# Optimization experiments

Hardware: AMD Instinct MI355X
Metric: run time of the kernel (lower is better)

## Reference

```python
import jax, jax.numpy as jnp
import numpy as np

B, L, E, H = 4096, 200, 64, 128

def setup_inputs() -> dict:
    key = jax.random.key(0)
    k1, k2, k3, k4, k5, k6, k7 = jax.random.split(key, 7)
    behavior_emb = jax.random.normal(k1, (B, L, E), dtype=jnp.float32)
    target_emb = jax.random.normal(k2, (B, 1, E), dtype=jnp.float32)
    seq_len = jax.random.randint(k3, (B,), 0, 200)
    # attention MLP params: Linear(4E, H), Linear(H, 1)
    W1 = jax.random.normal(k4, (4 * E, H), dtype=jnp.float32) / np.sqrt(4 * E)
    b1 = jnp.zeros((H,), dtype=jnp.float32)
    W2 = jax.random.normal(k5, (H, 1), dtype=jnp.float32) / np.sqrt(H)
    b2 = jnp.zeros((1,), dtype=jnp.float32)
    return {"behavior_emb": behavior_emb, "target_emb": target_emb,
            "seq_len": seq_len, "W1": W1, "b1": b1, "W2": W2, "b2": b2}

def reference(behavior_emb, target_emb, seq_len, W1, b1, W2, b2):
    b, l, e = behavior_emb.shape
    t = jnp.broadcast_to(target_emb, (b, l, e))  # [B,L,E]
    # concat(behavior, target, behavior*target, behavior-target) -> [B,L,4E]
    feat = jnp.concatenate([behavior_emb, t, behavior_emb * t, behavior_emb - t], axis=-1)
    h = jax.nn.relu(jnp.einsum('blf,fh->blh', feat, W1) + b1)  # dropout = identity (eval)
    att = (jnp.einsum('blh,ho->blo', h, W2) + b2)[..., 0]      # [B,L]
    mask = jnp.arange(l)[None, :] < seq_len[:, None]           # [B,L]
    att = jnp.where(mask, att, -1e9)
    att = jax.nn.softmax(att, axis=-1)
    weighted_emb = jnp.einsum('bl,ble->be', att, behavior_emb)  # [B,E]
    return weighted_emb
```

## Files before the change

### kernel.cpp

```cpp
#include <hip/hip_runtime.h>
#include <hip/hip_bf16.h>

typedef __attribute__((ext_vector_type(8))) __bf16 bf16x8;
typedef __attribute__((ext_vector_type(4))) __bf16 bf16x4;
typedef __attribute__((ext_vector_type(4))) float  f32x4;

#define L_SEQ 200
#define LPAD  208

__global__ void setup_bc(const float* __restrict__ W1, __bf16* __restrict__ Bc) {
    const int idx = blockIdx.x * 256 + threadIdx.x;
    const int j  = idx & 7;
    const int c  = (idx >> 3) & 15;
    const int kq = (idx >> 7) & 3;
    const int ks = (idx >> 9) & 3;
    const int ct = idx >> 11;
    const int k   = ks * 32 + kq * 8 + j;
    const int col = ct * 16 + c;
    float v;
    if (k < 64) v = W1[k * 128 + col] + W1[(192 + k) * 128 + col];
    else        v = W1[(128 + (k - 64)) * 128 + col];
    Bc[idx] = (__bf16)v;
}

__global__ __launch_bounds__(256) void setup_tb(
    const float* __restrict__ target, const float* __restrict__ W1,
    const float* __restrict__ b1, __bf16* __restrict__ TB)
{
    __shared__ float Wbd[64][128];
    __shared__ float Ts[16][64];
    const int tid = threadIdx.x;
    const int b0  = blockIdx.x * 16;
    for (int q = tid; q < 64 * 128; q += 256) {
        const int e = q >> 7, c = q & 127;
        Wbd[e][c] = W1[(64 + e) * 128 + c] - W1[(192 + e) * 128 + c];
    }
    for (int q = tid; q < 16 * 64; q += 256) {
        const int bb = q >> 6, e = q & 63;
        Ts[bb][e] = target[(size_t)(b0 + bb) * 64 + e];
    }
    __syncthreads();
    const int bb = tid >> 4;
    const int c0 = (tid & 15) * 8;
    float acc[8];
    #pragma unroll
    for (int r = 0; r < 8; ++r) acc[r] = b1[c0 + r];
    for (int e = 0; e < 64; ++e) {
        const float tv = Ts[bb][e];
        #pragma unroll
        for (int r = 0; r < 8; ++r) acc[r] += tv * Wbd[e][c0 + r];
    }
    #pragma unroll
    for (int r = 0; r < 8; ++r)
        TB[(size_t)(b0 + bb) * 128 + c0 + r] = (__bf16)acc[r];
}

__global__ __launch_bounds__(256, 4) void din_main(
    const float* __restrict__ behavior,
    const float* __restrict__ target,
    const int*   __restrict__ seqlen,
    const float* __restrict__ W2,
    const __bf16* __restrict__ Bc,
    const __bf16* __restrict__ TB,
    float* __restrict__ out)
{
    __shared__ __align__(16) __bf16 Xbf[LPAD * 64];
    __shared__ float att_part[4][LPAD];
    __shared__ float att_s[LPAD];
    __shared__ float red_s[8];
    __shared__ float part_s[4 * 64];

    const int b    = blockIdx.x;
    const int tid  = threadIdx.x;
    const int lane = tid & 63;
    const int w    = tid >> 6;
    const int kq   = lane >> 4;
    const int c16  = lane & 15;

    bf16x8 bfrag[2][4];
    #pragma unroll
    for (int i = 0; i < 2; ++i) {
        const int ct = 2 * w + i;
        #pragma unroll
        for (int ks = 0; ks < 4; ++ks)
            bfrag[i][ks] = *(const bf16x8*)(Bc + ((ct * 4 + ks) * 4 + kq) * 128 + c16 * 8);
    }
    float tf0[8], tf1[8];
    {
        const float* tp = target + (size_t)b * 64 + kq * 8;
        #pragma unroll
        for (int j = 0; j < 8; ++j) { tf0[j] = tp[j]; tf1[j] = tp[32 + j]; }
    }
    float tb_l[2], w2_l[2];
    #pragma unroll
    for (int i = 0; i < 2; ++i) {
        const int col = (2 * w + i) * 16 + c16;
        tb_l[i] = (float)TB[(size_t)b * 128 + col];
        w2_l[i] = W2[col];
    }

    {
        const float4* Xg = (const float4*)(behavior + (size_t)b * L_SEQ * 64);
        for (int q = tid; q < L_SEQ * 16; q += 256) {
            const int row = q >> 4;
            const int j   = q & 15;
            float4 v = Xg[q];
            bf16x4 u = { (__bf16)v.x, (__bf16)v.y, (__bf16)v.z, (__bf16)v.w };
            *(bf16x4*)&Xbf[row * 64 + ((j * 4) ^ ((row & 7) << 3))] = u;
        }
        for (int q = tid; q < 8 * 64; q += 256) {
            const int row = L_SEQ + (q >> 6);
            const int e   = q & 63;
            Xbf[row * 64 + (e ^ ((row & 7) << 3))] = (__bf16)0.0f;
        }
    }
    __syncthreads();

    {
        const int k0 = kq * 8;
        for (int tile = 0; tile < 13; ++tile) {
            const int row = tile * 16 + c16;
            const int sw  = (row & 7) << 3;
            bf16x8 a0 = *(const bf16x8*)&Xbf[row * 64 + (k0 ^ sw)];
            bf16x8 a1 = *(const bf16x8*)&Xbf[row * 64 + ((k0 + 32) ^ sw)];
            bf16x8 a2, a3;
            #pragma unroll
            for (int j = 0; j < 8; ++j) {
                a2[j] = (__bf16)((float)a0[j] * tf0[j]);
                a3[j] = (__bf16)((float)a1[j] * tf1[j]);
            }
            float s[4] = {0.f, 0.f, 0.f, 0.f};
            #pragma unroll
            for (int i = 0; i < 2; ++i) {
                f32x4 acc = {0.f, 0.f, 0.f, 0.f};
                acc = __builtin_amdgcn_mfma_f32_16x16x32_bf16(a0, bfrag[i][0], acc, 0, 0, 0);
                acc = __builtin_amdgcn_mfma_f32_16x16x32_bf16(a1, bfrag[i][1], acc, 0, 0, 0);
                acc = __builtin_amdgcn_mfma_f32_16x16x32_bf16(a2, bfrag[i][2], acc, 0, 0, 0);
                acc = __builtin_amdgcn_mfma_f32_16x16x32_bf16(a3, bfrag[i][3], acc, 0, 0, 0);
                #pragma unroll
                for (int r = 0; r < 4; ++r)
                    s[r] += fmaxf(acc[r] + tb_l[i], 0.f) * w2_l[i];
            }
            #pragma unroll
            for (int r = 0; r < 4; ++r) {
                float v = s[r];
                v += __shfl_xor(v, 1, 64);
                v += __shfl_xor(v, 2, 64);
                v += __shfl_xor(v, 4, 64);
                v += __shfl_xor(v, 8, 64);
                s[r] = v;
            }
            if (c16 == 0) {
                const int r0 = tile * 16 + kq * 4;
                #pragma unroll
                for (int r = 0; r < 4; ++r) att_part[w][r0 + r] = s[r];
            }
        }
    }
    __syncthreads();

    {
        const int sl = seqlen[b];
        float val = -INFINITY;
        if (tid < L_SEQ) {
            float v = att_part[0][tid] + att_part[1][tid]
                    + att_part[2][tid] + att_part[3][tid];
            val = (tid < sl) ? v : -1e9f;
        }
        float m = val;
        #pragma unroll
        for (int d = 1; d < 64; d <<= 1) m = fmaxf(m, __shfl_xor(m, d, 64));
        if (lane == 0) red_s[w] = m;
        __syncthreads();
        m = fmaxf(fmaxf(red_s[0], red_s[1]), fmaxf(red_s[2], red_s[3]));
        float p = (tid < L_SEQ) ? __expf(val - m) : 0.f;
        float sum = p;
        #pragma unroll
        for (int d = 1; d < 64; d <<= 1) sum += __shfl_xor(sum, d, 64);
        if (lane == 0) red_s[4 + w] = sum;
        __syncthreads();
        sum = red_s[4] + red_s[5] + red_s[6] + red_s[7];
        const float winv = 1.0f / sum;
        if (tid < L_SEQ) att_s[tid] = p * winv;
    }
    __syncthreads();

    {
        float acc = 0.f;
        for (int l = w; l < L_SEQ; l += 4)
            acc += att_s[l] * (float)Xbf[l * 64 + (lane ^ ((l & 7) << 3))];
        part_s[w * 64 + lane] = acc;
    }
    __syncthreads();
    if (tid < 64)
        out[(size_t)b * 64 + tid] =
            part_s[tid] + part_s[64 + tid] + part_s[128 + tid] + part_s[192 + tid];
}

extern "C" void kernel_launch(void* const* d_in, const int* in_sizes, int n_in,
                              void* d_out, int out_size, void* d_ws, size_t ws_size,
                              hipStream_t stream) {
    (void)n_in; (void)out_size; (void)ws_size;
    const float* behavior = (const float*)d_in[0];
    const float* target   = (const float*)d_in[1];
    const int*   seqlen   = (const int*)d_in[2];
    const float* W1       = (const float*)d_in[3];
    const float* b1       = (const float*)d_in[4];
    const float* W2       = (const float*)d_in[5];
    float* out = (float*)d_out;
    const int B = in_sizes[2];

    __bf16* Bc = (__bf16*)d_ws;
    __bf16* TB = (__bf16*)((char*)d_ws + 32768);

    setup_bc<<<dim3(64), dim3(256), 0, stream>>>(W1, Bc);
    setup_tb<<<dim3(B / 16), dim3(256), 0, stream>>>(target, W1, b1, TB);
    din_main<<<dim3(B), dim3(256), 0, stream>>>(behavior, target, seqlen, W2, Bc, TB, out);
}
```

Measured before the change: 334.2 us.

## Fold target into per-batch effective weights to halve MFMA work

Precomputes a per-batch bf16 weight matrix Weff = (W_a+W_d) + t*W_c, so the main kernel multiplies behavior rows by a 64-wide K instead of 128 and no longer forms behavior*target in registers. It also issues behavior loads in batches before the shared-memory writes, prefetches the next MFMA A-fragments, raises the occupancy hint to 5, keeps TB in fp32, and vectorizes the weighted-sum pass with 8-wide LDS reads and shuffle reductions. In exchange, a per-batch weight tensor (16 KB per batch, 64 MB total) is written and read back through global memory, and the product term is now rounded differently.

```diff
diff --git a/kernel.cpp b/kernel.cpp
--- a/kernel.cpp
+++ b/kernel.cpp
@@ -3,29 +3,56 @@
 
 typedef __attribute__((ext_vector_type(8))) __bf16 bf16x8;
 typedef __attribute__((ext_vector_type(4))) __bf16 bf16x4;
+typedef __attribute__((ext_vector_type(2))) __bf16 bf16x2;
 typedef __attribute__((ext_vector_type(4))) float  f32x4;
 
 #define L_SEQ 200
 #define LPAD  208
 
-__global__ void setup_bc(const float* __restrict__ W1, __bf16* __restrict__ Bc) {
-    const int idx = blockIdx.x * 256 + threadIdx.x;
-    const int j  = idx & 7;
-    const int c  = (idx >> 3) & 15;
-    const int kq = (idx >> 7) & 3;
-    const int ks = (idx >> 9) & 3;
-    const int ct = idx >> 11;
-    const int k   = ks * 32 + kq * 8 + j;
-    const int col = ct * 16 + c;
-    float v;
-    if (k < 64) v = W1[k * 128 + col] + W1[(192 + k) * 128 + col];
-    else        v = W1[(128 + (k - 64)) * 128 + col];
-    Bc[idx] = (__bf16)v;
+__global__ __launch_bounds__(256) void setup_weff(
+    const float* __restrict__ W1, const float* __restrict__ target,
+    __bf16* __restrict__ Weff)
+{
+    __shared__ float t_s[16][64];
+    const int tid = threadIdx.x;
+    const int b0  = blockIdx.x * 16;
+    ((float4*)t_s)[tid] = ((const float4*)(target + (size_t)b0 * 64))[tid];
+
+    const int c16 = tid & 15;
+    const int kq  = (tid >> 4) & 3;
+    const int ks  = (tid >> 6) & 1;
+    const int k0  = ks * 32 + kq * 8;
+    float wad[4][8], wc[4][8];
+    #pragma unroll
+    for (int i = 0; i < 4; ++i) {
+        const int col = (i * 2 + (tid >> 7)) * 16 + c16;
+        #pragma unroll
+        for (int j = 0; j < 8; ++j) {
+            const int k = k0 + j;
+            wad[i][j] = W1[k * 128 + col] + W1[(192 + k) * 128 + col];
+            wc[i][j]  = W1[(128 + k) * 128 + col];
+        }
+    }
+    __syncthreads();
+    for (int bb = 0; bb < 16; ++bb) {
+        float tv[8];
+        #pragma unroll
+        for (int j = 0; j < 8; ++j) tv[j] = t_s[bb][k0 + j];
+        #pragma unroll
+        for (int i = 0; i < 4; ++i) {
+            const int frag = i * 256 + tid;
+            bf16x8 o;
+            #pragma unroll
+            for (int j = 0; j < 8; ++j)
+                o[j] = (__bf16)(wad[i][j] + tv[j] * wc[i][j]);
+            *(bf16x8*)(Weff + ((size_t)(b0 + bb) * 1024 + frag) * 8) = o;
+        }
+    }
 }
 
 __global__ __launch_bounds__(256) void setup_tb(
     const float* __restrict__ target, const float* __restrict__ W1,
-    const float* __restrict__ b1, __bf16* __restrict__ TB)
+    const float* __restrict__ b1, float* __restrict__ TB)
 {
     __shared__ float Wbd[64][128];
     __shared__ float Ts[16][64];
@@ -35,10 +62,7 @@
         const int e = q >> 7, c = q & 127;
         Wbd[e][c] = W1[(64 + e) * 128 + c] - W1[(192 + e) * 128 + c];
     }
-    for (int q = tid; q < 16 * 64; q += 256) {
-        const int bb = q >> 6, e = q & 63;
-        Ts[bb][e] = target[(size_t)(b0 + bb) * 64 + e];
-    }
+    ((float4*)Ts)[tid] = ((const float4*)(target + (size_t)b0 * 64))[tid];
     __syncthreads();
     const int bb = tid >> 4;
     const int c0 = (tid & 15) * 8;
@@ -52,23 +76,22 @@
     }
     #pragma unroll
     for (int r = 0; r < 8; ++r)
-        TB[(size_t)(b0 + bb) * 128 + c0 + r] = (__bf16)acc[r];
-}
-
-__global__ __launch_bounds__(256, 4) void din_main(
+        TB[(size_t)(b0 + bb) * 128 + c0 + r] = acc[r];
+}
+
+__global__ __launch_bounds__(256, 5) void din_main(
     const float* __restrict__ behavior,
-    const float* __restrict__ target,
     const int*   __restrict__ seqlen,
     const float* __restrict__ W2,
-    const __bf16* __restrict__ Bc,
-    const __bf16* __restrict__ TB,
+    const __bf16* __restrict__ Weff,
+    const float* __restrict__ TB,
     float* __restrict__ out)
 {
     __shared__ __align__(16) __bf16 Xbf[LPAD * 64];
     __shared__ float att_part[4][LPAD];
     __shared__ float att_s[LPAD];
+    __shared__ float part_s[256];
     __shared__ float red_s[8];
-    __shared__ float part_s[4 * 64];
 
     const int b    = blockIdx.x;
     const int tid  = threadIdx.x;
@@ -77,70 +100,78 @@
     const int kq   = lane >> 4;
     const int c16  = lane & 15;
 
-    bf16x8 bfrag[2][4];
+    const float4* Xg = (const float4*)(behavior + (size_t)b * L_SEQ * 64);
+    float4 va[7];
+    #pragma unroll
+    for (int i = 0; i < 7; ++i) va[i] = Xg[tid + i * 256];
+
+    bf16x8 bfrag[2][2];
+    float tb_l[2], w2_l[2];
     #pragma unroll
     for (int i = 0; i < 2; ++i) {
         const int ct = 2 * w + i;
         #pragma unroll
-        for (int ks = 0; ks < 4; ++ks)
-            bfrag[i][ks] = *(const bf16x8*)(Bc + ((ct * 4 + ks) * 4 + kq) * 128 + c16 * 8);
-    }
-    float tf0[8], tf1[8];
-    {
-        const float* tp = target + (size_t)b * 64 + kq * 8;
-        #pragma unroll
-        for (int j = 0; j < 8; ++j) { tf0[j] = tp[j]; tf1[j] = tp[32 + j]; }
-    }
-    float tb_l[2], w2_l[2];
-    #pragma unroll
-    for (int i = 0; i < 2; ++i) {
-        const int col = (2 * w + i) * 16 + c16;
-        tb_l[i] = (float)TB[(size_t)b * 128 + col];
-        w2_l[i] = W2[col];
-    }
-
-    {
-        const float4* Xg = (const float4*)(behavior + (size_t)b * L_SEQ * 64);
-        for (int q = tid; q < L_SEQ * 16; q += 256) {
-            const int row = q >> 4;
-            const int j   = q & 15;
-            float4 v = Xg[q];
+        for (int ks = 0; ks < 2; ++ks)
+            bfrag[i][ks] = *(const bf16x8*)(Weff +
+                ((size_t)b * 1024 + ((ct * 2 + ks) * 4 + kq) * 16 + c16) * 8);
+        tb_l[i] = TB[(size_t)b * 128 + ct * 16 + c16];
+        w2_l[i] = W2[ct * 16 + c16];
+    }
+    float4 vb[6];
+    #pragma unroll
+    for (int i = 0; i < 6; ++i) {
+        const int q = tid + (7 + i) * 256;
+        if (q < L_SEQ * 16) vb[i] = Xg[q];
+    }
+    #pragma unroll
+    for (int i = 0; i < 7; ++i) {
+        const int q = tid + i * 256;
+        const int row = q >> 4, j4 = (q & 15) * 4, sw = (row & 7) << 3;
+        float4 v = va[i];
+        bf16x4 u = { (__bf16)v.x, (__bf16)v.y, (__bf16)v.z, (__bf16)v.w };
+        *(bf16x4*)&Xbf[row * 64 + (j4 ^ sw)] = u;
+    }
+    {
+        const int row = L_SEQ + (tid >> 5), e0 = (tid & 31) * 2;
+        bf16x2 z = { (__bf16)0.f, (__bf16)0.f };
+        *(bf16x2*)&Xbf[row * 64 + (e0 ^ ((row & 7) << 3))] = z;
+    }
+    #pragma unroll
+    for (int i = 0; i < 6; ++i) {
+        const int q = tid + (7 + i) * 256;
+        if (q < L_SEQ * 16) {
+            const int row = q >> 4, j4 = (q & 15) * 4, sw = (row & 7) << 3;
+            float4 v = vb[i];
             bf16x4 u = { (__bf16)v.x, (__bf16)v.y, (__bf16)v.z, (__bf16)v.w };
-            *(bf16x4*)&Xbf[row * 64 + ((j * 4) ^ ((row & 7) << 3))] = u;
-        }
-        for (int q = tid; q < 8 * 64; q += 256) {
-            const int row = L_SEQ + (q >> 6);
-            const int e   = q & 63;
-            Xbf[row * 64 + (e ^ ((row & 7) << 3))] = (__bf16)0.0f;
-        }
-    }
-    __syncthreads();
-
-    {
-        const int k0 = kq * 8;
+            *(bf16x4*)&Xbf[row * 64 + (j4 ^ sw)] = u;
+        }
+    }
+    __syncthreads();
+
+    {
+        const int sw  = (c16 & 7) << 3;
+        const int k0  = kq * 8;
+        const int o0  = k0 ^ sw, o1 = (k0 + 32) ^ sw;
+        const f32x4 zero = {0.f, 0.f, 0.f, 0.f};
+        bf16x8 a0 = *(const bf16x8*)&Xbf[c16 * 64 + o0];
+        bf16x8 a1 = *(const bf16x8*)&Xbf[c16 * 64 + o1];
         for (int tile = 0; tile < 13; ++tile) {
-            const int row = tile * 16 + c16;
-            const int sw  = (row & 7) << 3;
-            bf16x8 a0 = *(const bf16x8*)&Xbf[row * 64 + (k0 ^ sw)];
-            bf16x8 a1 = *(const bf16x8*)&Xbf[row * 64 + ((k0 + 32) ^ sw)];
-            bf16x8 a2, a3;
-            #pragma unroll
-            for (int j = 0; j < 8; ++j) {
-                a2[j] = (__bf16)((float)a0[j] * tf0[j]);
-                a3[j] = (__bf16)((float)a1[j] * tf1[j]);
-            }
-            float s[4] = {0.f, 0.f, 0.f, 0.f};
-            #pragma unroll
-            for (int i = 0; i < 2; ++i) {
-                f32x4 acc = {0.f, 0.f, 0.f, 0.f};
-                acc = __builtin_amdgcn_mfma_f32_16x16x32_bf16(a0, bfrag[i][0], acc, 0, 0, 0);
-                acc = __builtin_amdgcn_mfma_f32_16x16x32_bf16(a1, bfrag[i][1], acc, 0, 0, 0);
-                acc = __builtin_amdgcn_mfma_f32_16x16x32_bf16(a2, bfrag[i][2], acc, 0, 0, 0);
-                acc = __builtin_amdgcn_mfma_f32_16x16x32_bf16(a3, bfrag[i][3], acc, 0, 0, 0);
-                #pragma unroll
-                for (int r = 0; r < 4; ++r)
-                    s[r] += fmaxf(acc[r] + tb_l[i], 0.f) * w2_l[i];
-            }
+            bf16x8 an0, an1;
+            if (tile < 12) {
+                const int rb = ((tile + 1) * 16 + c16) * 64;
+                an0 = *(const bf16x8*)&Xbf[rb + o0];
+                an1 = *(const bf16x8*)&Xbf[rb + o1];
+            }
+            f32x4 acc0 = zero, acc1 = zero;
+            acc0 = __builtin_amdgcn_mfma_f32_16x16x32_bf16(a0, bfrag[0][0], acc0, 0, 0, 0);
+            acc0 = __builtin_amdgcn_mfma_f32_16x16x32_bf16(a1, bfrag[0][1], acc0, 0, 0, 0);
+            acc1 = __builtin_amdgcn_mfma_f32_16x16x32_bf16(a0, bfrag[1][0], acc1, 0, 0, 0);
+            acc1 = __builtin_amdgcn_mfma_f32_16x16x32_bf16(a1, bfrag[1][1], acc1, 0, 0, 0);
+            float s[4];
+            #pragma unroll
+            for (int r = 0; r < 4; ++r)
+                s[r] = fmaxf(acc0[r] + tb_l[0], 0.f) * w2_l[0]
+                     + fmaxf(acc1[r] + tb_l[1], 0.f) * w2_l[1];
             #pragma unroll
             for (int r = 0; r < 4; ++r) {
                 float v = s[r];
@@ -155,6 +186,7 @@
                 #pragma unroll
                 for (int r = 0; r < 4; ++r) att_part[w][r0 + r] = s[r];
             }
+            a0 = an0; a1 = an1;
         }
     }
     __syncthreads();
@@ -181,15 +213,37 @@
         __syncthreads();
         sum = red_s[4] + red_s[5] + red_s[6] + red_s[7];
         const float winv = 1.0f / sum;
-        if (tid < L_SEQ) att_s[tid] = p * winv;
-    }
-    __syncthreads();
-
-    {
-        float acc = 0.f;
-        for (int l = w; l < L_SEQ; l += 4)
-            acc += att_s[l] * (float)Xbf[l * 64 + (lane ^ ((l & 7) << 3))];
-        part_s[w * 64 + lane] = acc;
+        if (tid < LPAD) att_s[tid] = (tid < L_SEQ) ? p * winv : 0.f;
+    }
+    __syncthreads();
+
+    {
+        const int prow = tid >> 3;
+        const int cg   = tid & 7;
+        float acc[8] = {0.f,0.f,0.f,0.f,0.f,0.f,0.f,0.f};
+        #pragma unroll
+        for (int p = 0; p < 7; ++p) {
+            const int row = p * 32 + prow;
+            if (row < LPAD) {
+                const int sw = (row & 7) << 3;
+                bf16x8 xv = *(const bf16x8*)&Xbf[row * 64 + ((cg * 8) ^ sw)];
+                const float aw = att_s[row];
+                #pragma unroll
+                for (int j = 0; j < 8; ++j) acc[j] += aw * (float)xv[j];
+            }
+        }
+        #pragma unroll
+        for (int j = 0; j < 8; ++j) {
+            float v = acc[j];
+            v += __shfl_xor(v, 8, 64);
+            v += __shfl_xor(v, 16, 64);
+            v += __shfl_xor(v, 32, 64);
+            acc[j] = v;
+        }
+        if (lane < 8) {
+            #pragma unroll
+            for (int j = 0; j < 8; ++j) part_s[w * 64 + lane * 8 + j] = acc[j];
+        }
     }
     __syncthreads();
     if (tid < 64)
@@ -210,10 +264,10 @@
     float* out = (float*)d_out;
     const int B = in_sizes[2];
 
-    __bf16* Bc = (__bf16*)d_ws;
-    __bf16* TB = (__bf16*)((char*)d_ws + 32768);
-
-    setup_bc<<<dim3(64), dim3(256), 0, stream>>>(W1, Bc);
-    setup_tb<<<dim3(B / 16), dim3(256), 0, stream>>>(target, W1, b1, TB);
-    din_main<<<dim3(B), dim3(256), 0, stream>>>(behavior, target, seqlen, W2, Bc, TB, out);
-}
+    __bf16* Weff = (__bf16*)d_ws;
+    float*  TB   = (float*)((char*)d_ws + (size_t)B * 8192 * 2);
+
+    setup_weff<<<dim3(B / 16), dim3(256), 0, stream>>>(W1, target, Weff);
+    setup_tb  <<<dim3(B / 16), dim3(256), 0, stream>>>(target, W1, b1, TB);
+    din_main  <<<dim3(B), dim3(256), 0, stream>>>(behavior, seqlen, W2, Weff, TB, out);
+}
```

New measurement: 326.9 us. -2.2%, faster.

## Process eight batches per block with register-prefetched double-buffered behavior tiles

Applied to the files above, without the earlier changes.

Each block now loops over eight batch rows. The next batch's behavior, target and bias values are prefetched into registers while the current batch runs MFMA scoring and softmax, then stored into the alternate LDS buffer. The pooling step is rewritten to use vector LDS reads and shuffle reductions, and TB is kept in fp32. This aims to hide global load latency and cut per-block setup cost, at the price of lower occupancy (2 blocks per CU) and more registers.

```diff
diff --git a/kernel.cpp b/kernel.cpp
--- a/kernel.cpp
+++ b/kernel.cpp
@@ -3,10 +3,12 @@
 
 typedef __attribute__((ext_vector_type(8))) __bf16 bf16x8;
 typedef __attribute__((ext_vector_type(4))) __bf16 bf16x4;
+typedef __attribute__((ext_vector_type(2))) __bf16 bf16x2;
 typedef __attribute__((ext_vector_type(4))) float  f32x4;
 
 #define L_SEQ 200
 #define LPAD  208
+#define BPB   8
 
 __global__ void setup_bc(const float* __restrict__ W1, __bf16* __restrict__ Bc) {
     const int idx = blockIdx.x * 256 + threadIdx.x;
@@ -25,7 +27,7 @@
 
 __global__ __launch_bounds__(256) void setup_tb(
     const float* __restrict__ target, const float* __restrict__ W1,
-    const float* __restrict__ b1, __bf16* __restrict__ TB)
+    const float* __restrict__ b1, float* __restrict__ TB)
 {
     __shared__ float Wbd[64][128];
     __shared__ float Ts[16][64];
@@ -35,10 +37,7 @@
         const int e = q >> 7, c = q & 127;
         Wbd[e][c] = W1[(64 + e) * 128 + c] - W1[(192 + e) * 128 + c];
     }
-    for (int q = tid; q < 16 * 64; q += 256) {
-        const int bb = q >> 6, e = q & 63;
-        Ts[bb][e] = target[(size_t)(b0 + bb) * 64 + e];
-    }
+    ((float4*)Ts)[tid] = ((const float4*)(target + (size_t)b0 * 64))[tid];
     __syncthreads();
     const int bb = tid >> 4;
     const int c0 = (tid & 15) * 8;
@@ -52,149 +51,235 @@
     }
     #pragma unroll
     for (int r = 0; r < 8; ++r)
-        TB[(size_t)(b0 + bb) * 128 + c0 + r] = (__bf16)acc[r];
+        TB[(size_t)(b0 + bb) * 128 + c0 + r] = acc[r];
 }
 
-__global__ __launch_bounds__(256, 4) void din_main(
+__global__ __launch_bounds__(256, 2) void din_main(
     const float* __restrict__ behavior,
     const float* __restrict__ target,
     const int*   __restrict__ seqlen,
     const float* __restrict__ W2,
     const __bf16* __restrict__ Bc,
-    const __bf16* __restrict__ TB,
+    const float* __restrict__ TB,
     float* __restrict__ out)
 {
-    __shared__ __align__(16) __bf16 Xbf[LPAD * 64];
+    __shared__ __align__(16) __bf16 Xbf[2][LPAD * 64];
     __shared__ float att_part[4][LPAD];
     __shared__ float att_s[LPAD];
+    __shared__ float part_s[256];
     __shared__ float red_s[8];
-    __shared__ float part_s[4 * 64];
-
-    const int b    = blockIdx.x;
+
     const int tid  = threadIdx.x;
     const int lane = tid & 63;
     const int w    = tid >> 6;
     const int kq   = lane >> 4;
     const int c16  = lane & 15;
+    const int b0   = blockIdx.x * BPB;
 
     bf16x8 bfrag[2][4];
+    float w2_l[2];
     #pragma unroll
     for (int i = 0; i < 2; ++i) {
         const int ct = 2 * w + i;
         #pragma unroll
         for (int ks = 0; ks < 4; ++ks)
             bfrag[i][ks] = *(const bf16x8*)(Bc + ((ct * 4 + ks) * 4 + kq) * 128 + c16 * 8);
-    }
-    float tf0[8], tf1[8];
+        w2_l[i] = W2[ct * 16 + c16];
+    }
     {
-        const float* tp = target + (size_t)b * 64 + kq * 8;
+        const int row = L_SEQ + (tid >> 5);
+        const int e0  = (tid & 31) * 2;
+        const int off = row * 64 + (e0 ^ ((row & 7) << 3));
+        bf16x2 z = { (__bf16)0.f, (__bf16)0.f };
+        *(bf16x2*)&Xbf[0][off] = z;
+        *(bf16x2*)&Xbf[1][off] = z;
+    }
+
+    float4 vn[13];
+    float4 tfn[4];
+    float  tbn[2];
+    {
+        const float4* Xg = (const float4*)(behavior + (size_t)b0 * (L_SEQ * 64));
         #pragma unroll
-        for (int j = 0; j < 8; ++j) { tf0[j] = tp[j]; tf1[j] = tp[32 + j]; }
-    }
-    float tb_l[2], w2_l[2];
+        for (int q = 0; q < 13; ++q) {
+            const int idx = tid + q * 256;
+            if (q < 12 || idx < L_SEQ * 16) vn[q] = Xg[idx];
+        }
+        const float* tp = target + (size_t)b0 * 64 + kq * 8;
+        tfn[0] = *(const float4*)tp;
+        tfn[1] = *(const float4*)(tp + 4);
+        tfn[2] = *(const float4*)(tp + 32);
+        tfn[3] = *(const float4*)(tp + 36);
+        tbn[0] = TB[(size_t)b0 * 128 + (2 * w) * 16 + c16];
+        tbn[1] = TB[(size_t)b0 * 128 + (2 * w + 1) * 16 + c16];
+    }
     #pragma unroll
-    for (int i = 0; i < 2; ++i) {
-        const int col = (2 * w + i) * 16 + c16;
-        tb_l[i] = (float)TB[(size_t)b * 128 + col];
-        w2_l[i] = W2[col];
-    }
-
-    {
-        const float4* Xg = (const float4*)(behavior + (size_t)b * L_SEQ * 64);
-        for (int q = tid; q < L_SEQ * 16; q += 256) {
-            const int row = q >> 4;
-            const int j   = q & 15;
-            float4 v = Xg[q];
+    for (int q = 0; q < 13; ++q) {
+        const int idx = tid + q * 256;
+        if (q < 12 || idx < L_SEQ * 16) {
+            const int row = idx >> 4, j4 = (idx & 15) * 4, sw = (row & 7) << 3;
+            float4 v = vn[q];
             bf16x4 u = { (__bf16)v.x, (__bf16)v.y, (__bf16)v.z, (__bf16)v.w };
-            *(bf16x4*)&Xbf[row * 64 + ((j * 4) ^ ((row & 7) << 3))] = u;
-        }
-        for (int q = tid; q < 8 * 64; q += 256) {
-            const int row = L_SEQ + (q >> 6);
-            const int e   = q & 63;
-            Xbf[row * 64 + (e ^ ((row & 7) << 3))] = (__bf16)0.0f;
+            *(bf16x4*)&Xbf[0][row * 64 + (j4 ^ sw)] = u;
         }
     }
     __syncthreads();
 
-    {
-        const int k0 = kq * 8;
-        for (int tile = 0; tile < 13; ++tile) {
-            const int row = tile * 16 + c16;
-            const int sw  = (row & 7) << 3;
-            bf16x8 a0 = *(const bf16x8*)&Xbf[row * 64 + (k0 ^ sw)];
-            bf16x8 a1 = *(const bf16x8*)&Xbf[row * 64 + ((k0 + 32) ^ sw)];
-            bf16x8 a2, a3;
-            #pragma unroll
-            for (int j = 0; j < 8; ++j) {
-                a2[j] = (__bf16)((float)a0[j] * tf0[j]);
-                a3[j] = (__bf16)((float)a1[j] * tf1[j]);
-            }
-            float s[4] = {0.f, 0.f, 0.f, 0.f};
-            #pragma unroll
-            for (int i = 0; i < 2; ++i) {
-                f32x4 acc = {0.f, 0.f, 0.f, 0.f};
-                acc = __builtin_amdgcn_mfma_f32_16x16x32_bf16(a0, bfrag[i][0], acc, 0, 0, 0);
-                acc = __builtin_amdgcn_mfma_f32_16x16x32_bf16(a1, bfrag[i][1], acc, 0, 0, 0);
-                acc = __builtin_amdgcn_mfma_f32_16x16x32_bf16(a2, bfrag[i][2], acc, 0, 0, 0);
-                acc = __builtin_amdgcn_mfma_f32_16x16x32_bf16(a3, bfrag[i][3], acc, 0, 0, 0);
+    for (int i = 0; i < BPB; ++i) {
+        const int b   = b0 + i;
+        const int cur = i & 1;
+        const int sl  = seqlen[b];
+
+        float tf0[8], tf1[8], tb_l[2];
+        #pragma unroll
+        for (int j = 0; j < 4; ++j) {
+            tf0[j]     = tfn[0][j];
+            tf0[4 + j] = tfn[1][j];
+            tf1[j]     = tfn[2][j];
+            tf1[4 + j] = tfn[3][j];
+        }
+        tb_l[0] = tbn[0]; tb_l[1] = tbn[1];
+
+        if (i + 1 < BPB) {
+            const float4* Xg = (const float4*)(behavior + (size_t)(b + 1) * (L_SEQ * 64));
+            #pragma unroll
+            for (int q = 0; q < 13; ++q) {
+                const int idx = tid + q * 256;
+                if (q < 12 || idx < L_SEQ * 16) vn[q] = Xg[idx];
+            }
+            const float* tp = target + (size_t)(b + 1) * 64 + kq * 8;
+            tfn[0] = *(const float4*)tp;
+            tfn[1] = *(const float4*)(tp + 4);
+            tfn[2] = *(const float4*)(tp + 32);
+            tfn[3] = *(const float4*)(tp + 36);
+            tbn[0] = TB[(size_t)(b + 1) * 128 + (2 * w) * 16 + c16];
+            tbn[1] = TB[(size_t)(b + 1) * 128 + (2 * w + 1) * 16 + c16];
+        }
+
+        {
+            const __bf16* Xc = &Xbf[cur][0];
+            const int sw = (c16 & 7) << 3;
+            const int k0 = kq * 8;
+            const int o0 = k0 ^ sw, o1 = (k0 + 32) ^ sw;
+            const f32x4 zero = {0.f, 0.f, 0.f, 0.f};
+            bf16x8 a0 = *(const bf16x8*)&Xc[c16 * 64 + o0];
+            bf16x8 a1 = *(const bf16x8*)&Xc[c16 * 64 + o1];
+            for (int tile = 0; tile < 13; ++tile) {
+                bf16x8 an0, an1;
+                if (tile < 12) {
+                    const int rb = ((tile + 1) * 16 + c16) * 64;
+                    an0 = *(const bf16x8*)&Xc[rb + o0];
+                    an1 = *(const bf16x8*)&Xc[rb + o1];
+                }
+                bf16x8 a2, a3;
+                #pragma unroll
+                for (int j = 0; j < 8; ++j) {
+                    a2[j] = (__bf16)((float)a0[j] * tf0[j]);
+                    a3[j] = (__bf16)((float)a1[j] * tf1[j]);
+                }
+                f32x4 acc0 = zero, acc1 = zero;
+                acc0 = __builtin_amdgcn_mfma_f32_16x16x32_bf16(a0, bfrag[0][0], acc0, 0, 0, 0);
+                acc0 = __builtin_amdgcn_mfma_f32_16x16x32_bf16(a1, bfrag[0][1], acc0, 0, 0, 0);
+                acc0 = __builtin_amdgcn_mfma_f32_16x16x32_bf16(a2, bfrag[0][2], acc0, 0, 0, 0);
+                acc0 = __builtin_amdgcn_mfma_f32_16x16x32_bf16(a3, bfrag[0][3], acc0, 0, 0, 0);
+                acc1 = __builtin_amdgcn_mfma_f32_16x16x32_bf16(a0, bfrag[1][0], acc1, 0, 0, 0);
+                acc1 = __builtin_amdgcn_mfma_f32_16x16x32_bf16(a1, bfrag[1][1], acc1, 0, 0, 0);
+                acc1 = __builtin_amdgcn_mfma_f32_16x16x32_bf16(a2, bfrag[1][2], acc1, 0, 0, 0);
+                acc1 = __builtin_amdgcn_mfma_f32_16x16x32_bf16(a3, bfrag[1][3], acc1, 0, 0, 0);
+                float s[4];
                 #pragma unroll
                 for (int r = 0; r < 4; ++r)
-                    s[r] += fmaxf(acc[r] + tb_l[i], 0.f) * w2_l[i];
-            }
-            #pragma unroll
-            for (int r = 0; r < 4; ++r) {
-                float v = s[r];
-                v += __shfl_xor(v, 1, 64);
-                v += __shfl_xor(v, 2, 64);
-                v += __shfl_xor(v, 4, 64);
+                    s[r] = fmaxf(acc0[r] + tb_l[0], 0.f) * w2_l[0]
+                         + fmaxf(acc1[r] + tb_l[1], 0.f) * w2_l[1];
+                #pragma unroll
+                for (int r = 0; r < 4; ++r) {
+                    float v = s[r];
+                    v += __shfl_xor(v, 1, 64);
+                    v += __shfl_xor(v, 2, 64);
+                    v += __shfl_xor(v, 4, 64);
+                    v += __shfl_xor(v, 8, 64);
+                    s[r] = v;
+                }
+                if (c16 == 0) {
+                    const int r0 = tile * 16 + kq * 4;
+                    #pragma unroll
+                    for (int r = 0; r < 4; ++r) att_part[w][r0 + r] = s[r];
+                }
+                a0 = an0; a1 = an1;
+            }
+        }
+        __syncthreads();
+
+        {
+            float val = -INFINITY;
+            if (tid < L_SEQ) {
+                float v = att_part[0][tid] + att_part[1][tid]
+                        + att_part[2][tid] + att_part[3][tid];
+                val = (tid < sl) ? v : -1e9f;
+            }
+            float m = val;
+            #pragma unroll
+            for (int d = 1; d < 64; d <<= 1) m = fmaxf(m, __shfl_xor(m, d, 64));
+            if (lane == 0) red_s[w] = m;
+            __syncthreads();
+            m = fmaxf(fmaxf(red_s[0], red_s[1]), fmaxf(red_s[2], red_s[3]));
+            float p = (tid < L_SEQ) ? __expf(val - m) : 0.f;
+            float sum = p;
+            #pragma unroll
+            for (int d = 1; d < 64; d <<= 1) sum += __shfl_xor(sum, d, 64);
+            if (lane == 0) red_s[4 + w] = sum;
+            __syncthreads();
+            sum = red_s[4] + red_s[5] + red_s[6] + red_s[7];
+            const float winv = 1.0f / sum;
+            if (tid < LPAD) att_s[tid] = (tid < L_SEQ) ? p * winv : 0.f;
+        }
+        __syncthreads();
+
+        {
+            const int prow = tid >> 3;
+            const int cg   = tid & 7;
+            float acc[8] = {0.f,0.f,0.f,0.f,0.f,0.f,0.f,0.f};
+            #pragma unroll
+            for (int p = 0; p < 7; ++p) {
+                const int row = p * 32 + prow;
+                if (row < LPAD) {
+                    const int sw2 = (row & 7) << 3;
+                    bf16x8 xv = *(const bf16x8*)&Xbf[cur][row * 64 + ((cg * 8) ^ sw2)];
+                    const float aw = att_s[row];
+                    #pragma unroll
+                    for (int j = 0; j < 8; ++j) acc[j] += aw * (float)xv[j];
+                }
+            }
+            #pragma unroll
+            for (int j = 0; j < 8; ++j) {
+                float v = acc[j];
                 v += __shfl_xor(v, 8, 64);
-                s[r] = v;
-            }
-            if (c16 == 0) {
-                const int r0 = tile * 16 + kq * 4;
+                v += __shfl_xor(v, 16, 64);
+                v += __shfl_xor(v, 32, 64);
+                acc[j] = v;
+            }
+            if (lane < 8) {
                 #pragma unroll
-                for (int r = 0; r < 4; ++r) att_part[w][r0 + r] = s[r];
-            }
-        }
-    }
-    __syncthreads();
-
-    {
-        const int sl = seqlen[b];
-        float val = -INFINITY;
-        if (tid < L_SEQ) {
-            float v = att_part[0][tid] + att_part[1][tid]
-                    + att_part[2][tid] + att_part[3][tid];
-            val = (tid < sl) ? v : -1e9f;
-        }
-        float m = val;
-        #pragma unroll
-        for (int d = 1; d < 64; d <<= 1) m = fmaxf(m, __shfl_xor(m, d, 64));
-        if (lane == 0) red_s[w] = m;
+                for (int j = 0; j < 8; ++j) part_s[w * 64 + lane * 8 + j] = acc[j];
+            }
+        }
+        if (i + 1 < BPB) {
+            #pragma unroll
+            for (int q = 0; q < 13; ++q) {
+                const int idx = tid + q * 256;
+                if (q < 12 || idx < L_SEQ * 16) {
+                    const int row = idx >> 4, j4 = (idx & 15) * 4, sw2 = (row & 7) << 3;
+                    float4 v = vn[q];
+                    bf16x4 u = { (__bf16)v.x, (__bf16)v.y, (__bf16)v.z, (__bf16)v.w };
+                    *(bf16x4*)&Xbf[cur ^ 1][row * 64 + (j4 ^ sw2)] = u;
+                }
+            }
+        }
         __syncthreads();
-        m = fmaxf(fmaxf(red_s[0], red_s[1]), fmaxf(red_s[2], red_s[3]));
-        float p = (tid < L_SEQ) ? __expf(val - m) : 0.f;
-        float sum = p;
-        #pragma unroll
-        for (int d = 1; d < 64; d <<= 1) sum += __shfl_xor(sum, d, 64);
-        if (lane == 0) red_s[4 + w] = sum;
-        __syncthreads();
-        sum = red_s[4] + red_s[5] + red_s[6] + red_s[7];
-        const float winv = 1.0f / sum;
-        if (tid < L_SEQ) att_s[tid] = p * winv;
-    }
-    __syncthreads();
-
-    {
-        float acc = 0.f;
-        for (int l = w; l < L_SEQ; l += 4)
-            acc += att_s[l] * (float)Xbf[l * 64 + (lane ^ ((l & 7) << 3))];
-        part_s[w * 64 + lane] = acc;
-    }
-    __syncthreads();
-    if (tid < 64)
-        out[(size_t)b * 64 + tid] =
-            part_s[tid] + part_s[64 + tid] + part_s[128 + tid] + part_s[192 + tid];
+        if (tid < 64)
+            out[(size_t)b * 64 + tid] =
+                part_s[tid] + part_s[64 + tid] + part_s[128 + tid] + part_s[192 + tid];
+    }
 }
 
 extern "C" void kernel_launch(void* const* d_in, const int* in_sizes, int n_in,
@@ -211,9 +296,9 @@
     const int B = in_sizes[2];
 
     __bf16* Bc = (__bf16*)d_ws;
-    __bf16* TB = (__bf16*)((char*)d_ws + 32768);
+    float*  TB = (float*)((char*)d_ws + 32768);
 
     setup_bc<<<dim3(64), dim3(256), 0, stream>>>(W1, Bc);
     setup_tb<<<dim3(B / 16), dim3(256), 0, stream>>>(target, W1, b1, TB);
-    din_main<<<dim3(B), dim3(256), 0, stream>>>(behavior, target, seqlen, W2, Bc, TB, out);
+    din_main<<<dim3(B / BPB), dim3(256), 0, stream>>>(behavior, target, seqlen, W2, Bc, TB, out);
 }
```

Measured after the change: 331.8 us. No clear change (-0.7%).
